# Kernel tuning notes

Hardware: AMD Instinct MI355X
Metric: run time of the kernel (lower is better)

## Reference

```python
import jax, jax.numpy as jnp
import numpy as np

C_IN = 128
D_K = 256
D_V = 256
N_HEAD = 8
H = 192
W = 192
REGION = 3
TEMPER = int(np.sqrt(D_K))  # int(sqrt(d_k)) per the torch module


def setup_inputs() -> dict:
    key = jax.random.key(0)
    k1, k2, k3, k4 = jax.random.split(key, 4)
    scale = 1.0 / np.sqrt(C_IN).astype(np.float32)
    x = jax.random.normal(k1, (1, C_IN, H, W), dtype=jnp.float32)
    wq = jax.random.normal(k2, (D_K, C_IN), dtype=jnp.float32) * scale
    wk = jax.random.normal(k3, (D_K, C_IN), dtype=jnp.float32) * scale
    wv = jax.random.normal(k4, (D_V, C_IN), dtype=jnp.float32) * scale
    return {"x": x, "wq": wq, "wk": wk, "wv": wv}


def _stretch(t):
    # Equivalent of the fixed Conv3d 'stretch' trick: for each (i, j) in the
    # 3x3 region, channel 3*i+j holds the input shifted by (i-1, j-1), zero-padded.
    # t: [b, d, H, W] -> [b, 9, d, H, W]
    b, d, h, w = t.shape
    tp = jnp.pad(t, ((0, 0), (0, 0), (1, 1), (1, 1)))
    return jnp.stack(
        [tp[:, :, i:i + h, j:j + w] for i in range(REGION) for j in range(REGION)],
        axis=1,
    )


def reference(x, wq, wk, wv):
    b = x.shape[0]  # must be 1 (module's broadcast only works for batch 1)
    dkh = D_K // N_HEAD
    dvh = D_V // N_HEAD
    r2 = REGION * REGION
    # 1x1 conv projections == channel matmuls
    q = jnp.einsum('oc,bchw->bohw', wq, x)
    k = jnp.einsum('oc,bchw->bohw', wk, x)
    v = jnp.einsum('oc,bchw->bohw', wv, x)
    Q = _stretch(q)  # [b, 9, d_k, H, W]
    K = _stretch(k)
    V = _stretch(v)  # [b, 9, d_v, H, W]
    # elementwise QK, per-head channel sum, scale, softmax over the 9 region slots
    qk = (Q * K).reshape(b, r2, N_HEAD, dkh, H, W)
    scores = jax.nn.softmax(qk.sum(axis=3) / TEMPER, axis=1)  # [b, 9, n_head, H, W]
    # dropout is identity in eval mode (att_drop disabled for the reference)
    Vh = V.reshape(b, r2, N_HEAD, dvh, H, W)
    out = (scores[:, :, :, None] * Vh).sum(axis=1).reshape(b, D_V, H, W)
    return out
```

## Files before the change

### kernel.cpp

```cpp
#include <hip/hip_runtime.h>

#define HW_   36864
#define WI    192
#define HT    192
#define CIN   128
#define DK    256
#define NH    8
#define DKH   32

using short4_ = __attribute__((ext_vector_type(4))) short;
using short8  = __attribute__((ext_vector_type(8))) short;
using float4_ = __attribute__((ext_vector_type(4))) float;

static __device__ __forceinline__ float b2f(unsigned short u) {
    union { unsigned int i; float f; } x; x.i = ((unsigned int)u) << 16; return x.f;
}
static __device__ __forceinline__ unsigned short f2b(float f) {
    union { float f; unsigned int i; } x; x.f = f;
    unsigned int r = x.i + 0x7FFFu + ((x.i >> 16) & 1u);
    return (unsigned short)(r >> 16);
}

__global__ __launch_bounds__(256) void detect_kernel(
    const unsigned int* __restrict__ xw, int* __restrict__ flag)
{
    __shared__ int sh[256];
    int t = threadIdx.x;
    int cnt = 0;
    for (int i = t; i < 4096; i += 256) {
        unsigned int w = xw[i];
        unsigned int e = (w >> 23) & 0xFF;
        if (e >= 96 && e <= 160) cnt++;
    }
    sh[t] = cnt;
    __syncthreads();
    for (int s = 128; s > 0; s >>= 1) {
        if (t < s) sh[t] += sh[t + s];
        __syncthreads();
    }
    if (t == 0) *flag = (sh[0] > 2048) ? 1 : 0;
}

__global__ __launch_bounds__(256) void convw_kernel(
    const void* __restrict__ wq,
    const void* __restrict__ wk,
    const void* __restrict__ wv,
    const int* __restrict__ flag,
    unsigned short* __restrict__ wqkv)
{
    int id = blockIdx.x * 256 + threadIdx.x;
    int h   = id / 12288;
    int rem = id - h * 12288;
    int r   = rem >> 7;
    int c   = rem & 127;
    const void* s = (r < 32) ? wq : ((r < 64) ? wk : wv);
    int si = (h * 32 + (r & 31)) * 128 + c;
    if (*flag) wqkv[id] = f2b(((const float*)s)[si]);
    else       wqkv[id] = ((const unsigned short*)s)[si];
}

__global__ __launch_bounds__(256) void convx_kernel(
    const void* __restrict__ x, const int* __restrict__ flag,
    unsigned short* __restrict__ xt)
{
    __shared__ unsigned short tile[64][136];
    const int px0 = blockIdx.x * 64;
    const int t = threadIdx.x;
    if (*flag) {
        const float* __restrict__ xf = (const float*)x;
        for (int i = 0; i < 32; ++i) {
            int id = i * 256 + t;
            int c = id >> 6, p = id & 63;
            tile[p][c] = f2b(xf[c * HW_ + px0 + p]);
        }
    } else {
        const unsigned short* __restrict__ xb = (const unsigned short*)x;
        for (int i = 0; i < 32; ++i) {
            int id = i * 256 + t;
            int c = id >> 6, p = id & 63;
            tile[p][c] = xb[c * HW_ + px0 + p];
        }
    }
    __syncthreads();
    for (int i = 0; i < 4; ++i) {
        int id = i * 256 + t;
        int row = id >> 4, c8 = id & 15;
        *(short8*)&xt[(px0 + row) * 128 + c8 * 8] =
            *(const short8*)&tile[row][c8 * 8];
    }
}

__global__ __launch_bounds__(256) void projmm_kernel(
    const unsigned short* __restrict__ xt,
    const unsigned short* __restrict__ wqkv,
    unsigned short* __restrict__ vbuf,
    float* __restrict__ sbuf)
{
    __shared__ unsigned short As[96 * 136];
    __shared__ unsigned short Bs[128 * 136];
    const int head = blockIdx.x;
    const int px0  = blockIdx.y * 128;
    const int t = threadIdx.x;

    const unsigned short* __restrict__ Ag = wqkv + head * 96 * 128;
    #pragma unroll
    for (int i = 0; i < 6; ++i) {
        int id = i * 256 + t;
        int row = id >> 4, c8 = id & 15;
        *(short8*)&As[row * 136 + c8 * 8] = *(const short8*)&Ag[row * 128 + c8 * 8];
    }
    const unsigned short* __restrict__ Bg = xt + px0 * 128;
    #pragma unroll
    for (int i = 0; i < 8; ++i) {
        int id = i * 256 + t;
        int row = id >> 4, c8 = id & 15;
        *(short8*)&Bs[row * 136 + c8 * 8] = *(const short8*)&Bg[row * 128 + c8 * 8];
    }
    __syncthreads();

    const int lane = t & 63, wave = t >> 6;
    const int col = lane & 15, quad = lane >> 4;

    short8 bfrag[2][4];
    #pragma unroll
    for (int nt = 0; nt < 2; ++nt)
        #pragma unroll
        for (int kt = 0; kt < 4; ++kt) {
            int n = wave * 32 + nt * 16 + col;
            bfrag[nt][kt] = *(const short8*)&Bs[n * 136 + kt * 32 + quad * 8];
        }

    float4_ acc[6][2];
    #pragma unroll
    for (int mt = 0; mt < 6; ++mt)
        #pragma unroll
        for (int nt = 0; nt < 2; ++nt)
            acc[mt][nt] = (float4_){0.f, 0.f, 0.f, 0.f};

    #pragma unroll
    for (int mt = 0; mt < 6; ++mt) {
        #pragma unroll
        for (int kt = 0; kt < 4; ++kt) {
            int m = mt * 16 + col;
            short8 a = *(const short8*)&As[m * 136 + kt * 32 + quad * 8];
            acc[mt][0] = __builtin_amdgcn_mfma_f32_16x16x32_bf16(a, bfrag[0][kt], acc[mt][0], 0, 0, 0);
            acc[mt][1] = __builtin_amdgcn_mfma_f32_16x16x32_bf16(a, bfrag[1][kt], acc[mt][1], 0, 0, 0);
        }
    }

    #pragma unroll
    for (int nt = 0; nt < 2; ++nt) {
        int px = px0 + wave * 32 + nt * 16 + col;
        float s = 0.f;
        #pragma unroll
        for (int reg = 0; reg < 4; ++reg)
            s += acc[0][nt][reg] * acc[2][nt][reg]
               + acc[1][nt][reg] * acc[3][nt][reg];
        s += __shfl_xor(s, 16, 64);
        s += __shfl_xor(s, 32, 64);
        if (quad == 0) sbuf[head * HW_ + px] = s;
        unsigned short* vp = vbuf + ((size_t)head * HW_ + px) * 32;
        short4_ v0, v1;
        #pragma unroll
        for (int reg = 0; reg < 4; ++reg) {
            v0[reg] = (short)f2b(acc[4][nt][reg]);
            v1[reg] = (short)f2b(acc[5][nt][reg]);
        }
        *(short4_*)&vp[quad * 4]      = v0;
        *(short4_*)&vp[16 + quad * 4] = v1;
    }
}

__global__ __launch_bounds__(256) void attn_kernel(
    const unsigned short* __restrict__ vbuf,
    const float* __restrict__ sbuf,
    const int* __restrict__ flag,
    void* __restrict__ out)
{
    __shared__ float tr[32][65];
    const int b    = blockIdx.x;
    const int tile = b % 576;
    const int head = b / 576;
    const int t    = threadIdx.x;
    const int pxl  = t >> 2;
    const int cg   = t & 3;
    const int px   = tile * 64 + pxl;
    const int y    = px / WI;
    const int xx   = px - y * WI;
    const bool f32 = (*flag != 0);

    const float* __restrict__ Sh = sbuf + head * HW_;

    float w[9];
    int   np[9];
    float m = -1e30f;
    #pragma unroll
    for (int r = 0; r < 9; ++r) {
        int dy = r / 3 - 1, dx = r % 3 - 1;
        int ny = y + dy, nx = xx + dx;
        bool inb = (ny >= 0) && (ny < HT) && (nx >= 0) && (nx < WI);
        int idx = inb ? (ny * WI + nx) : px;
        np[r] = idx;
        float val = inb ? (Sh[idx] * 0.0625f) : 0.0f;
        w[r] = val;
        m = fmaxf(m, val);
    }
    float wsum = 0.f;
    #pragma unroll
    for (int r = 0; r < 9; ++r) {
        float e = __expf(w[r] - m);
        w[r] = e;
        wsum += e;
    }
    float inv = 1.0f / wsum;
    #pragma unroll
    for (int r = 0; r < 9; ++r) {
        int dy = r / 3 - 1, dx = r % 3 - 1;
        int ny = y + dy, nx = xx + dx;
        bool inb = (ny >= 0) && (ny < HT) && (nx >= 0) && (nx < WI);
        w[r] = inb ? (w[r] * inv) : 0.0f;
    }

    const unsigned short* __restrict__ vb = vbuf + (size_t)head * HW_ * 32;
    float acc[8] = {0.f, 0.f, 0.f, 0.f, 0.f, 0.f, 0.f, 0.f};
    #pragma unroll
    for (int r = 0; r < 9; ++r) {
        short8 v8 = *(const short8*)&vb[np[r] * 32 + cg * 8];
        #pragma unroll
        for (int j = 0; j < 8; ++j)
            acc[j] = fmaf(w[r], b2f((unsigned short)v8[j]), acc[j]);
    }
    #pragma unroll
    for (int j = 0; j < 8; ++j)
        tr[cg * 8 + j][pxl] = acc[j];
    __syncthreads();

    const int ch = t >> 3, c8 = t & 7;
    const int px0 = tile * 64;
    const size_t obase = (size_t)(head * DKH + ch) * HW_ + px0 + c8 * 8;
    if (f32) {
        float4_ o0, o1;
        #pragma unroll
        for (int j = 0; j < 4; ++j) {
            o0[j] = tr[ch][c8 * 8 + j];
            o1[j] = tr[ch][c8 * 8 + 4 + j];
        }
        float* o = (float*)out + obase;
        *(float4_*)&o[0] = o0;
        *(float4_*)&o[4] = o1;
    } else {
        short8 o8;
        #pragma unroll
        for (int j = 0; j < 8; ++j)
            o8[j] = (short)f2b(tr[ch][c8 * 8 + j]);
        *(short8*)((unsigned short*)out + obase) = o8;
    }
}

extern "C" void kernel_launch(void* const* d_in, const int* in_sizes, int n_in,
                              void* d_out, int out_size, void* d_ws, size_t ws_size,
                              hipStream_t stream) {
    const void* x  = d_in[0];
    const void* wq = d_in[1];
    const void* wk = d_in[2];
    const void* wv = d_in[3];

    char* ws = (char*)d_ws;
    int*            flag = (int*)ws;
    unsigned short* wqkv = (unsigned short*)(ws + 256);
    unsigned short* xt   = (unsigned short*)(ws + 196864);
    unsigned short* vbuf = (unsigned short*)(ws + 9634048);
    float*          sbuf = (float*)(ws + 28508416);

    detect_kernel<<<1, 256, 0, stream>>>((const unsigned int*)x, flag);
    convw_kernel<<<384, 256, 0, stream>>>(wq, wk, wv, flag, wqkv);
    convx_kernel<<<576, 256, 0, stream>>>(x, flag, xt);
    projmm_kernel<<<dim3(8, 288), 256, 0, stream>>>(xt, wqkv, vbuf, sbuf);
    attn_kernel<<<4608, 256, 0, stream>>>(vbuf, sbuf, flag, (void*)d_out);
}
```

Before: 120.3 us.

## Fuse dtype detection and conversion kernels; drop LDS staging in projection GEMM

The separate detect, weight-convert and input-convert kernels are merged into one launch. Every block now repeats the dtype vote itself, using a wave-shuffle reduction, and one extra block converts the weights serially. The projection GEMM no longer stages A and B tiles through shared memory and loads MFMA fragments straight from global memory. This removes two launches and a barrier, but adds redundant vote reads in every block, a long serial tail for the single weight block, and uncoalesced fragment loads that depend on the cache.

After: 260.5 us. +116.6%, slower.

```diff
diff --git a/kernel.cpp b/kernel.cpp
--- a/kernel.cpp
+++ b/kernel.cpp
@@ -21,52 +21,51 @@
     return (unsigned short)(r >> 16);
 }
 
-__global__ __launch_bounds__(256) void detect_kernel(
-    const unsigned int* __restrict__ xw, int* __restrict__ flag)
-{
-    __shared__ int sh[256];
-    int t = threadIdx.x;
+static __device__ __forceinline__ bool vote_f32(const unsigned int* xw, int t,
+                                                int* votes ) {
     int cnt = 0;
     for (int i = t; i < 4096; i += 256) {
-        unsigned int w = xw[i];
-        unsigned int e = (w >> 23) & 0xFF;
-        if (e >= 96 && e <= 160) cnt++;
-    }
-    sh[t] = cnt;
+        unsigned int e = (xw[i] >> 23) & 0xFF;
+        cnt += (e >= 96 && e <= 160) ? 1 : 0;
+    }
+    #pragma unroll
+    for (int o = 32; o > 0; o >>= 1) cnt += __shfl_down(cnt, o, 64);
+    if ((t & 63) == 0) votes[t >> 6] = cnt;
     __syncthreads();
-    for (int s = 128; s > 0; s >>= 1) {
-        if (t < s) sh[t] += sh[t + s];
-        __syncthreads();
-    }
-    if (t == 0) *flag = (sh[0] > 2048) ? 1 : 0;
-}
-
-__global__ __launch_bounds__(256) void convw_kernel(
+    return (votes[0] + votes[1] + votes[2] + votes[3]) > 2048;
+}
+
+__global__ __launch_bounds__(256) void convxw_kernel(
+    const void* __restrict__ x,
     const void* __restrict__ wq,
     const void* __restrict__ wk,
     const void* __restrict__ wv,
-    const int* __restrict__ flag,
-    unsigned short* __restrict__ wqkv)
-{
-    int id = blockIdx.x * 256 + threadIdx.x;
-    int h   = id / 12288;
-    int rem = id - h * 12288;
-    int r   = rem >> 7;
-    int c   = rem & 127;
-    const void* s = (r < 32) ? wq : ((r < 64) ? wk : wv);
-    int si = (h * 32 + (r & 31)) * 128 + c;
-    if (*flag) wqkv[id] = f2b(((const float*)s)[si]);
-    else       wqkv[id] = ((const unsigned short*)s)[si];
-}
-
-__global__ __launch_bounds__(256) void convx_kernel(
-    const void* __restrict__ x, const int* __restrict__ flag,
-    unsigned short* __restrict__ xt)
+    unsigned short* __restrict__ xt,
+    unsigned short* __restrict__ wqkv,
+    int* __restrict__ flag)
 {
     __shared__ unsigned short tile[64][136];
+    __shared__ int votes[4];
+    const int t = threadIdx.x;
+    const bool f32 = vote_f32((const unsigned int*)x, t, votes);
+
+    if (blockIdx.x == 576) {
+        if (t == 0) *flag = f32 ? 1 : 0;
+        for (int i = t; i < 98304; i += 256) {
+            int h   = i / 12288;
+            int rem = i - h * 12288;
+            int r   = rem >> 7;
+            int c   = rem & 127;
+            const void* s = (r < 32) ? wq : ((r < 64) ? wk : wv);
+            int si = (h * 32 + (r & 31)) * 128 + c;
+            wqkv[i] = f32 ? f2b(((const float*)s)[si])
+                          : ((const unsigned short*)s)[si];
+        }
+        return;
+    }
+
     const int px0 = blockIdx.x * 64;
-    const int t = threadIdx.x;
-    if (*flag) {
+    if (f32) {
         const float* __restrict__ xf = (const float*)x;
         for (int i = 0; i < 32; ++i) {
             int id = i * 256 + t;
@@ -96,30 +95,14 @@
     unsigned short* __restrict__ vbuf,
     float* __restrict__ sbuf)
 {
-    __shared__ unsigned short As[96 * 136];
-    __shared__ unsigned short Bs[128 * 136];
     const int head = blockIdx.x;
     const int px0  = blockIdx.y * 128;
-    const int t = threadIdx.x;
+    const int t    = threadIdx.x;
+    const int lane = t & 63, wave = t >> 6;
+    const int col  = lane & 15, quad = lane >> 4;
 
     const unsigned short* __restrict__ Ag = wqkv + head * 96 * 128;
-    #pragma unroll
-    for (int i = 0; i < 6; ++i) {
-        int id = i * 256 + t;
-        int row = id >> 4, c8 = id & 15;
-        *(short8*)&As[row * 136 + c8 * 8] = *(const short8*)&Ag[row * 128 + c8 * 8];
-    }
-    const unsigned short* __restrict__ Bg = xt + px0 * 128;
-    #pragma unroll
-    for (int i = 0; i < 8; ++i) {
-        int id = i * 256 + t;
-        int row = id >> 4, c8 = id & 15;
-        *(short8*)&Bs[row * 136 + c8 * 8] = *(const short8*)&Bg[row * 128 + c8 * 8];
-    }
-    __syncthreads();
-
-    const int lane = t & 63, wave = t >> 6;
-    const int col = lane & 15, quad = lane >> 4;
+    const unsigned short* __restrict__ Bg = xt + (size_t)px0 * 128;
 
     short8 bfrag[2][4];
     #pragma unroll
@@ -127,7 +110,7 @@
         #pragma unroll
         for (int kt = 0; kt < 4; ++kt) {
             int n = wave * 32 + nt * 16 + col;
-            bfrag[nt][kt] = *(const short8*)&Bs[n * 136 + kt * 32 + quad * 8];
+            bfrag[nt][kt] = *(const short8*)&Bg[n * 128 + kt * 32 + quad * 8];
         }
 
     float4_ acc[6][2];
@@ -141,8 +124,7 @@
     for (int mt = 0; mt < 6; ++mt) {
         #pragma unroll
         for (int kt = 0; kt < 4; ++kt) {
-            int m = mt * 16 + col;
-            short8 a = *(const short8*)&As[m * 136 + kt * 32 + quad * 8];
+            short8 a = *(const short8*)&Ag[(mt * 16 + col) * 128 + kt * 32 + quad * 8];
             acc[mt][0] = __builtin_amdgcn_mfma_f32_16x16x32_bf16(a, bfrag[0][kt], acc[mt][0], 0, 0, 0);
             acc[mt][1] = __builtin_amdgcn_mfma_f32_16x16x32_bf16(a, bfrag[1][kt], acc[mt][1], 0, 0, 0);
         }
@@ -272,9 +254,7 @@
     unsigned short* vbuf = (unsigned short*)(ws + 9634048);
     float*          sbuf = (float*)(ws + 28508416);
 
-    detect_kernel<<<1, 256, 0, stream>>>((const unsigned int*)x, flag);
-    convw_kernel<<<384, 256, 0, stream>>>(wq, wk, wv, flag, wqkv);
-    convx_kernel<<<576, 256, 0, stream>>>(x, flag, xt);
+    convxw_kernel<<<577, 256, 0, stream>>>(x, wq, wk, wv, xt, wqkv, flag);
     projmm_kernel<<<dim3(8, 288), 256, 0, stream>>>(xt, wqkv, vbuf, sbuf);
     attn_kernel<<<4608, 256, 0, stream>>>(vbuf, sbuf, flag, (void*)d_out);
 }
```
